# Kernel optimization log

Hardware: AMD Instinct MI355X
Metric: run time of the kernel (lower is better)

## Reference

```python
import jax, jax.numpy as jnp
import numpy as np

B, DEC_T, ENC_T = 64, 128, 1024
H, ENC_D, ATTN, VOCAB = 512, 512, 512, 128


def setup_inputs() -> dict:
    key = jax.random.key(0)
    ks = jax.random.split(key, 12)
    s = 0.05
    return {
        "inputs": jax.random.randint(ks[0], (B, DEC_T), 0, 127),
        "encoder_outputs": jax.random.normal(ks[1], (B, ENC_T, ENC_D), jnp.float32),
        "embedding": jax.random.normal(ks[2], (VOCAB, H), jnp.float32) * s,
        "w_ih": jax.random.normal(ks[3], (3 * H, H + ENC_D), jnp.float32) * s,
        "w_hh": jax.random.normal(ks[4], (3 * H, H), jnp.float32) * s,
        "b_ih": jnp.zeros((3 * H,), jnp.float32),
        "b_hh": jnp.zeros((3 * H,), jnp.float32),
        "attn_wq": jax.random.normal(ks[5], (ATTN, H), jnp.float32) * s,
        "attn_wv": jax.random.normal(ks[6], (ATTN, ENC_D), jnp.float32) * s,
        "attn_conv_w": jax.random.normal(ks[7], (ATTN, 1, 3), jnp.float32) * s,
        "attn_conv_b": jnp.zeros((ATTN,), jnp.float32),
        "attn_bias": jnp.zeros((ATTN,), jnp.float32),
        "attn_v": jax.random.normal(ks[8], (ATTN,), jnp.float32) * s,
        "fc_w": jax.random.normal(ks[9], (VOCAB, H + ENC_D), jnp.float32) * s,
        "fc_b": jnp.zeros((VOCAB,), jnp.float32),
    }


def reference(inputs, encoder_outputs, embedding, w_ih, w_hh, b_ih, b_hh,
              attn_wq, attn_wv, attn_conv_w, attn_conv_b, attn_bias, attn_v,
              fc_w, fc_b):
    emb = embedding[inputs]  # (B, dec_T, H); no eos in inputs so filter is identity
    # precompute encoder value projection once (reused every step)
    enc_proj = jnp.einsum('bte,ae->bta', encoder_outputs, attn_wv)  # (B, enc_T, A)

    def gru_step(h, x):
        gi = x @ w_ih.T + b_ih  # (B, 3H)
        gh = h @ w_hh.T + b_hh
        r = jax.nn.sigmoid(gi[:, :H] + gh[:, :H])
        z = jax.nn.sigmoid(gi[:, H:2 * H] + gh[:, H:2 * H])
        n = jnp.tanh(gi[:, 2 * H:] + r * gh[:, 2 * H:])
        return (1.0 - z) * n + z * h

    def step(carry, x_t):
        h, context, attn_w = carry
        rnn_in = jnp.concatenate([x_t, context], axis=1)  # (B, H+enc_D)
        h = gru_step(h, rnn_in)  # output == new hidden for 1-layer GRU
        # location-aware attention: conv over previous attention weights
        conv = jax.lax.conv_general_dilated(
            attn_w[:, None, :], attn_conv_w, (1,), ((1, 1),),
            dimension_numbers=('NCH', 'OIH', 'NCH'))  # (B, A, enc_T)
        conv_feat = conv.transpose(0, 2, 1) + attn_conv_b  # (B, enc_T, A)
        q = h @ attn_wq.T  # (B, A)
        e = jnp.tanh(q[:, None, :] + enc_proj + conv_feat + attn_bias)
        score = jnp.einsum('bta,a->bt', e, attn_v)  # (B, enc_T)
        attn_w = jax.nn.softmax(score, axis=-1)
        context = jnp.einsum('bt,bte->be', attn_w, encoder_outputs)  # (B, enc_D)
        out_cat = jnp.concatenate([h, context], axis=1)  # (B, H+enc_D)
        pred = jax.nn.log_softmax(out_cat @ fc_w.T + fc_b, axis=-1)  # (B, V)
        return (h, context, attn_w), (pred, attn_w, out_cat)

    init = (jnp.zeros((B, H), emb.dtype),
            jnp.zeros((B, ENC_D), emb.dtype),
            jnp.zeros((B, ENC_T), emb.dtype))
    _, (y, aw, oc) = jax.lax.scan(step, init, emb.transpose(1, 0, 2))
    # back to batch-major: (B, dec_T, *)
    return (y.transpose(1, 0, 2), aw.transpose(1, 0, 2), oc.transpose(1, 0, 2))
```

## Files before the change

kernel.cpp:

```cpp
#include <hip/hip_runtime.h>
#include <stdint.h>

#define BB 64
#define SS 128
#define EE 1024
#define HH 512
#define DD 512
#define AA 512
#define VV 128
#define KX 1536
#define NC 2048

#define AW_OFF ((size_t)BB*SS*VV)
#define OC_OFF (AW_OFF + (size_t)BB*SS*EE)

typedef unsigned short u16;

__device__ __forceinline__ float sigmoid_f(float x){
  return __builtin_amdgcn_rcpf(1.f + __expf(-x));
}
__device__ __forceinline__ float tanh_f(float x){
  float e = __expf(2.f*x);
  return 1.f - 2.f*__builtin_amdgcn_rcpf(e + 1.f);
}
__device__ __forceinline__ u16 f2bf(float f){
  uint32_t u = __float_as_uint(f);
  return (u16)((u + 0x7fffu + ((u>>16)&1u)) >> 16);
}

__global__ void k_build(const float* __restrict__ w_ih, const float* __restrict__ w_hh,
                        const float* __restrict__ b_ih, const float* __restrict__ b_hh,
                        const float* __restrict__ wq,   const float* __restrict__ wv,
                        const float* __restrict__ fc_w,
                        float* __restrict__ Wbig, float* __restrict__ wqT,
                        float* __restrict__ wvT,  float* __restrict__ fcT,
                        float* __restrict__ bias_big){
  int i = blockIdx.x*256 + threadIdx.x;
  const int NW = KX*NC;
  if (i < NW){
    int k = i >> 11, c = i & (NC-1);
    float v;
    if (c < 1024)      v = (k < 1024) ? w_ih[c*1024 + k] : w_hh[c*512 + (k-1024)];
    else if (c < 1536) v = (k < 1024) ? w_ih[c*1024 + k] : 0.f;
    else               v = (k >= 1024) ? w_hh[(c-512)*512 + (k-1024)] : 0.f;
    Wbig[i] = v; return;
  }
  i -= NW;
  if (i < 512*512){ int j = i >> 9, a = i & 511; wqT[i] = wq[a*512 + j]; return; }
  i -= 512*512;
  if (i < 512*512){ int e = i >> 9, a = i & 511; wvT[i] = wv[a*512 + e]; return; }
  i -= 512*512;
  if (i < 1024*128){ int k = i >> 7, v = i & 127; fcT[i] = fc_w[v*1024 + k]; return; }
  i -= 1024*128;
  if (i < NC){
    float bv;
    if (i < 1024)      bv = b_ih[i] + b_hh[i];
    else if (i < 1536) bv = b_ih[i];
    else               bv = b_hh[i - 512];
    bias_big[i] = bv;
  }
}

__global__ __launch_bounds__(256) void k_encp(const float* __restrict__ enc,
                                              const float* __restrict__ wvT,
                                              const float* __restrict__ abias,
                                              const float* __restrict__ convb,
                                              u16* __restrict__ encp){
  __shared__ float As[64][36];
  __shared__ float Bs[32][68];
  int tid = threadIdx.x;
  int r0 = blockIdx.x * 64;
  int a0 = blockIdx.y * 64;
  float4 acc[4];
  #pragma unroll
  for (int r = 0; r < 4; ++r) acc[r] = make_float4(0.f,0.f,0.f,0.f);
  int rl = tid >> 2, kl0 = (tid & 3) * 8;
  int kl2 = tid >> 3, al0 = (tid & 7) * 8;
  int br = (tid >> 4) * 4, cc = (tid & 15) * 4;
  for (int kk = 0; kk < 512; kk += 32){
    float4 av0 = *(const float4*)&enc[(size_t)(r0+rl)*512 + kk + kl0];
    float4 av1 = *(const float4*)&enc[(size_t)(r0+rl)*512 + kk + kl0 + 4];
    float4 bv0 = *(const float4*)&wvT[(size_t)(kk+kl2)*512 + a0 + al0];
    float4 bv1 = *(const float4*)&wvT[(size_t)(kk+kl2)*512 + a0 + al0 + 4];
    __syncthreads();
    *(float4*)&As[rl][kl0]     = av0;
    *(float4*)&As[rl][kl0+4]   = av1;
    *(float4*)&Bs[kl2][al0]    = bv0;
    *(float4*)&Bs[kl2][al0+4]  = bv1;
    __syncthreads();
    #pragma unroll
    for (int i = 0; i < 32; ++i){
      float4 b4 = *(const float4*)&Bs[i][cc];
      float x0 = As[br][i], x1 = As[br+1][i], x2 = As[br+2][i], x3 = As[br+3][i];
      acc[0].x += x0*b4.x; acc[0].y += x0*b4.y; acc[0].z += x0*b4.z; acc[0].w += x0*b4.w;
      acc[1].x += x1*b4.x; acc[1].y += x1*b4.y; acc[1].z += x1*b4.z; acc[1].w += x1*b4.w;
      acc[2].x += x2*b4.x; acc[2].y += x2*b4.y; acc[2].z += x2*b4.z; acc[2].w += x2*b4.w;
      acc[3].x += x3*b4.x; acc[3].y += x3*b4.y; acc[3].z += x3*b4.z; acc[3].w += x3*b4.w;
    }
  }
  int a = a0 + cc;
  float b0f = abias[a]   + convb[a];
  float b1f = abias[a+1] + convb[a+1];
  float b2f_ = abias[a+2] + convb[a+2];
  float b3f = abias[a+3] + convb[a+3];
  #pragma unroll
  for (int r = 0; r < 4; ++r){
    size_t row = (size_t)(r0 + br + r);
    ushort4 pk;
    pk.x = f2bf(acc[r].x + b0f);
    pk.y = f2bf(acc[r].y + b1f);
    pk.z = f2bf(acc[r].z + b2f_);
    pk.w = f2bf(acc[r].w + b3f);
    *(ushort4*)&encp[row*512 + a] = pk;
  }
}

__global__ __launch_bounds__(256) void k_encbf(const float* __restrict__ enc,
                                               u16* __restrict__ enc_bf){
  size_t i = ((size_t)blockIdx.x*256 + threadIdx.x) * 4;
  float4 v = *(const float4*)&enc[i];
  ushort4 pk;
  pk.x = f2bf(v.x); pk.y = f2bf(v.y); pk.z = f2bf(v.z); pk.w = f2bf(v.w);
  *(ushort4*)&enc_bf[i] = pk;
}

__global__ __launch_bounds__(256) void k_ggemm_fc(const int* __restrict__ inputs,
                                                  const float* __restrict__ emb,
                                                  const float* __restrict__ ctxp,
                                                  const float* __restrict__ h,
                                                  const float* __restrict__ Wbig,
                                                  float* __restrict__ Gp,
                                                  const float* __restrict__ fcT,
                                                  const float* __restrict__ fc_b,
                                                  float* __restrict__ out,
                                                  int s, int gemm_nb, int sfc){
  int tid = threadIdx.x;
  if ((int)blockIdx.x < gemm_nb){
    __shared__ float Xs[64][36];
    __shared__ float Ws[32][68];
    int bid = blockIdx.x;
    int c0 = (bid & 31) * 64;
    int kc = bid >> 5;
    int kbase = kc * 192;
    float4 acc[4];
    #pragma unroll
    for (int r = 0; r < 4; ++r) acc[r] = make_float4(0.f,0.f,0.f,0.f);
    int bl = tid >> 2, kl0 = (tid & 3) * 8;
    int kw = tid >> 3, cl0 = (tid & 7) * 8;
    int br = (tid >> 4) * 4, cc = (tid & 15) * 4;
    const float* emb_b = emb + (size_t)inputs[bl*SS + s]*HH;
    bool t0 = (s == 0);
    for (int kk = 0; kk < 192; kk += 32){
      float xv[8];
      #pragma unroll
      for (int u = 0; u < 8; ++u){
        int kg = kbase + kk + kl0 + u;
        float v;
        if (kg < 512)       v = emb_b[kg];
        else if (kg < 1024){
          if (t0) v = 0.f;
          else {
            int d = kg - 512;
            v = ctxp[(size_t)(0*64+bl)*512 + d] + ctxp[(size_t)(1*64+bl)*512 + d]
              + ctxp[(size_t)(2*64+bl)*512 + d] + ctxp[(size_t)(3*64+bl)*512 + d];
          }
        }
        else                v = t0 ? 0.f : h[bl*512 + kg - 1024];
        xv[u] = v;
      }
      float4 w1 = *(const float4*)&Wbig[(size_t)(kbase+kk+kw)*NC + c0 + cl0];
      float4 w2 = *(const float4*)&Wbig[(size_t)(kbase+kk+kw)*NC + c0 + cl0 + 4];
      __syncthreads();
      *(float4*)&Xs[bl][kl0]   = make_float4(xv[0],xv[1],xv[2],xv[3]);
      *(float4*)&Xs[bl][kl0+4] = make_float4(xv[4],xv[5],xv[6],xv[7]);
      *(float4*)&Ws[kw][cl0]   = w1;
      *(float4*)&Ws[kw][cl0+4] = w2;
      __syncthreads();
      #pragma unroll
      for (int i = 0; i < 32; ++i){
        float4 b4 = *(const float4*)&Ws[i][cc];
        float x0 = Xs[br][i], x1 = Xs[br+1][i], x2 = Xs[br+2][i], x3 = Xs[br+3][i];
        acc[0].x += x0*b4.x; acc[0].y += x0*b4.y; acc[0].z += x0*b4.z; acc[0].w += x0*b4.w;
        acc[1].x += x1*b4.x; acc[1].y += x1*b4.y; acc[1].z += x1*b4.z; acc[1].w += x1*b4.w;
        acc[2].x += x2*b4.x; acc[2].y += x2*b4.y; acc[2].z += x2*b4.z; acc[2].w += x2*b4.w;
        acc[3].x += x3*b4.x; acc[3].y += x3*b4.y; acc[3].z += x3*b4.z; acc[3].w += x3*b4.w;
      }
    }
    #pragma unroll
    for (int r = 0; r < 4; ++r)
      *(float4*)&Gp[(size_t)(kc*64 + br + r)*NC + c0 + cc] = acc[r];
  } else {
    if (sfc < 0) return;
    __shared__ float oc_l[1024];
    __shared__ float lp[2][128];
    __shared__ float l_l[128];
    int b = blockIdx.x - gemm_nb;
    oc_l[tid]       = h[b*512 + tid];
    oc_l[tid + 256] = h[b*512 + tid + 256];
    int d0 = tid*2;
    float a0 = 0.f, a1 = 0.f;
    #pragma unroll
    for (int cc2 = 0; cc2 < 4; ++cc2){
      float2 p2 = *(const float2*)&ctxp[(size_t)(cc2*64 + b)*512 + d0];
      a0 += p2.x; a1 += p2.y;
    }
    oc_l[512 + d0]     = a0;
    oc_l[512 + d0 + 1] = a1;
    size_t oco = OC_OFF + (size_t)(b*SS + sfc)*1024 + 512 + d0;
    out[oco]     = a0;
    out[oco + 1] = a1;
    __syncthreads();
    int v = tid & 127, half = tid >> 7;
    float acc = 0.f;
    #pragma unroll 8
    for (int k = 0; k < 512; ++k)
      acc += oc_l[half*512 + k] * fcT[(size_t)(half*512 + k)*128 + v];
    lp[half][v] = acc;
    __syncthreads();
    if (tid < 128) l_l[tid] = lp[0][tid] + lp[1][tid] + fc_b[tid];
    __syncthreads();
    if (tid < 128){
      float m = -1e30f;
      for (int i = 0; i < 128; ++i) m = fmaxf(m, l_l[i]);
      float sm = 0.f;
      for (int i = 0; i < 128; ++i) sm += __expf(l_l[i] - m);
      out[(size_t)(b*SS + sfc)*VV + tid] = l_l[tid] - m - __logf(sm);
    }
  }
}

__global__ __launch_bounds__(256) void k_gate_q(const float* __restrict__ Gp,
                                                const float* __restrict__ bias_big,
                                                float* __restrict__ h,
                                                const float* __restrict__ wqT,
                                                float* __restrict__ qp,
                                                float* __restrict__ out, int s){
  __shared__ float h_l[512];
  int tid = threadIdx.x;
  int jt = blockIdx.x, bt = blockIdx.y;
  bool t0 = (s == 0);
  #pragma unroll
  for (int it = 0; it < 2; ++it){
    int item = tid + it*256;
    int bi = item >> 6, jl = item & 63;
    int b = bt*8 + bi, j = jt*64 + jl;
    float s0=0.f, s1=0.f, s2=0.f, s3=0.f;
    #pragma unroll
    for (int kc = 0; kc < 8; ++kc){
      const float* g = Gp + (size_t)(kc*64 + b)*NC;
      s0 += g[j]; s1 += g[512+j]; s2 += g[1024+j]; s3 += g[1536+j];
    }
    float r = sigmoid_f(s0 + bias_big[j]);
    float z = sigmoid_f(s1 + bias_big[512+j]);
    float n = tanh_f(s2 + bias_big[1024+j] + r*(s3 + bias_big[1536+j]));
    float hold = t0 ? 0.f : h[b*512 + j];
    float hn = (1.f - z)*n + z*hold;
    h_l[item] = hn;
    h[b*512 + j] = hn;
    out[OC_OFF + (size_t)(b*SS + s)*1024 + j] = hn;
  }
  __syncthreads();
  int a0 = tid*2;
  float2 acc8[8];
  #pragma unroll
  for (int bi = 0; bi < 8; ++bi) acc8[bi] = make_float2(0.f, 0.f);
  for (int j = 0; j < 64; ++j){
    float2 w = *(const float2*)&wqT[(size_t)(jt*64 + j)*512 + a0];
    #pragma unroll
    for (int bi = 0; bi < 8; ++bi){
      float hv = h_l[bi*64 + j];
      acc8[bi].x += hv*w.x; acc8[bi].y += hv*w.y;
    }
  }
  #pragma unroll
  for (int bi = 0; bi < 8; ++bi)
    *(float2*)&qp[(size_t)(jt*64 + bt*8 + bi)*512 + a0] = acc8[bi];
}

__global__ __launch_bounds__(1024) void k_score(const float* __restrict__ qp,
                                                const float* __restrict__ attn_v,
                                                const float* __restrict__ conv_w,
                                                const u16* __restrict__ encp,
                                                const float* __restrict__ out_aw,
                                                float* __restrict__ score, int s){
  __shared__ float q_l[512], v_l[512], c0_l[512], c1_l[512], c2_l[512];
  int tid = threadIdx.x;
  int b = blockIdx.y, et = blockIdx.x;
  if (tid < 512){
    float qq = 0.f;
    #pragma unroll
    for (int jt = 0; jt < 8; ++jt) qq += qp[(size_t)(jt*64 + b)*512 + tid];
    q_l[tid]  = qq;
    v_l[tid]  = attn_v[tid];
    c0_l[tid] = conv_w[tid*3 + 0];
    c1_l[tid] = conv_w[tid*3 + 1];
    c2_l[tid] = conv_w[tid*3 + 2];
  }
  __syncthreads();
  int wave = tid >> 6, lane = tid & 63;
  float q8[8], v8[8], c08[8], c18[8], c28[8];
  #pragma unroll
  for (int i = 0; i < 8; ++i){
    int a = lane*8 + i;
    q8[i] = q_l[a]; v8[i] = v_l[a]; c08[i] = c0_l[a]; c18[i] = c1_l[a]; c28[i] = c2_l[a];
  }
  const float* awrow = out_aw + AW_OFF + (size_t)(b*SS + (s-1))*EE;
  #pragma unroll
  for (int eu = 0; eu < 8; ++eu){
    int e = et*128 + wave*8 + eu;
    float wl = 0.f, wc = 0.f, wr = 0.f;
    if (s > 0){
      wc = awrow[e];
      wl = (e > 0)    ? awrow[e-1] : 0.f;
      wr = (e < EE-1) ? awrow[e+1] : 0.f;
    }
    uint4 pk = *(const uint4*)(encp + ((size_t)(b*EE + e)*512 + lane*8));
    uint32_t ua[4] = {pk.x, pk.y, pk.z, pk.w};
    float acc = 0.f;
    #pragma unroll
    for (int p = 0; p < 4; ++p){
      float plo = __uint_as_float(ua[p] << 16);
      float phi = __uint_as_float(ua[p] & 0xffff0000u);
      int i = p*2;
      float v0 = q8[i]   + plo + c08[i]*wl   + c18[i]*wc   + c28[i]*wr;
      acc += tanh_f(v0) * v8[i];
      float v1 = q8[i+1] + phi + c08[i+1]*wl + c18[i+1]*wc + c28[i+1]*wr;
      acc += tanh_f(v1) * v8[i+1];
    }
    #pragma unroll
    for (int off = 32; off; off >>= 1) acc += __shfl_xor(acc, off, 64);
    if (lane == 0) score[b*EE + e] = acc;
  }
}

__global__ __launch_bounds__(512) void k_soft_ctx(const float* __restrict__ score,
                                                  const u16* __restrict__ enc_bf,
                                                  float* __restrict__ ctxp,
                                                  float* __restrict__ out, int s){
  __shared__ float s_l[1024];
  __shared__ float red[512];
  __shared__ float w_l[256];
  __shared__ float redc[8][512];
  int tid = threadIdx.x;
  int c = blockIdx.x, b = blockIdx.y;
  float lv0 = score[b*EE + tid];
  float lv1 = score[b*EE + 512 + tid];
  s_l[tid] = lv0; s_l[512 + tid] = lv1;
  float m = fmaxf(lv0, lv1);
  red[tid] = m; __syncthreads();
  for (int st = 256; st > 0; st >>= 1){
    if (tid < st) red[tid] = fmaxf(red[tid], red[tid+st]);
    __syncthreads();
  }
  m = red[0]; __syncthreads();
  float sm = __expf(lv0 - m) + __expf(lv1 - m);
  red[tid] = sm; __syncthreads();
  for (int st = 256; st > 0; st >>= 1){
    if (tid < st) red[tid] += red[tid+st];
    __syncthreads();
  }
  float rS = __builtin_amdgcn_rcpf(red[0]);
  if (tid < 256){
    int e = c*256 + tid;
    float w = __expf(s_l[e] - m) * rS;
    w_l[tid] = w;
    out[AW_OFF + (size_t)(b*SS + s)*EE + e] = w;
  }
  __syncthreads();
  int es = tid >> 6, lane = tid & 63;
  int d0 = lane * 8;
  float acc8[8];
  #pragma unroll
  for (int i = 0; i < 8; ++i) acc8[i] = 0.f;
  #pragma unroll 4
  for (int i = 0; i < 32; ++i){
    int e_loc = es*32 + i;
    int e = c*256 + e_loc;
    uint4 pk = *(const uint4*)(enc_bf + ((size_t)b*EE + e)*512 + d0);
    float w = w_l[e_loc];
    uint32_t ua[4] = {pk.x, pk.y, pk.z, pk.w};
    #pragma unroll
    for (int p = 0; p < 4; ++p){
      acc8[p*2]   += w * __uint_as_float(ua[p] << 16);
      acc8[p*2+1] += w * __uint_as_float(ua[p] & 0xffff0000u);
    }
  }
  #pragma unroll
  for (int i = 0; i < 8; ++i) redc[es][d0 + i] = acc8[i];
  __syncthreads();
  if (tid < 128){
    int d = tid * 4;
    float4 t = make_float4(0.f,0.f,0.f,0.f);
    #pragma unroll
    for (int e2 = 0; e2 < 8; ++e2){
      float4 r4 = *(const float4*)&redc[e2][d];
      t.x += r4.x; t.y += r4.y; t.z += r4.z; t.w += r4.w;
    }
    *(float4*)&ctxp[(size_t)(c*64 + b)*512 + d] = t;
  }
}

extern "C" void kernel_launch(void* const* d_in, const int* in_sizes, int n_in,
                              void* d_out, int out_size, void* d_ws, size_t ws_size,
                              hipStream_t stream){
  (void)in_sizes; (void)n_in; (void)out_size; (void)ws_size;
  const int*   inputs = (const int*)d_in[0];
  const float* enc    = (const float*)d_in[1];
  const float* emb    = (const float*)d_in[2];
  const float* w_ih   = (const float*)d_in[3];
  const float* w_hh   = (const float*)d_in[4];
  const float* b_ih   = (const float*)d_in[5];
  const float* b_hh   = (const float*)d_in[6];
  const float* wq     = (const float*)d_in[7];
  const float* wv     = (const float*)d_in[8];
  const float* convw  = (const float*)d_in[9];
  const float* convb  = (const float*)d_in[10];
  const float* abias  = (const float*)d_in[11];
  const float* av     = (const float*)d_in[12];
  const float* fcw    = (const float*)d_in[13];
  const float* fcb    = (const float*)d_in[14];
  float* out = (float*)d_out;

  char* p = (char*)d_ws;
  auto alloc = [&](size_t bytes)->char*{
    char* r = p; p += (bytes + 255) & ~(size_t)255; return r;
  };
  u16*   encp   = (u16*)  alloc((size_t)BB*EE*AA*2);
  u16*   enc_bf = (u16*)  alloc((size_t)BB*EE*DD*2);
  float* Wbig   = (float*)alloc((size_t)KX*NC*4);
  float* wqT    = (float*)alloc((size_t)512*512*4);
  float* wvT    = (float*)alloc((size_t)512*512*4);
  float* fcT    = (float*)alloc((size_t)1024*128*4);
  float* biasb  = (float*)alloc((size_t)NC*4);
  float* hbuf   = (float*)alloc((size_t)BB*HH*4);
  float* Gp     = (float*)alloc((size_t)8*BB*NC*4);
  float* qp     = (float*)alloc((size_t)8*BB*AA*4);
  float* score  = (float*)alloc((size_t)BB*EE*4);
  float* ctxp   = (float*)alloc((size_t)4*BB*DD*4);

  int total0 = KX*NC + 512*512 + 512*512 + 1024*128 + NC;
  k_build<<<(total0 + 255)/256, 256, 0, stream>>>(w_ih, w_hh, b_ih, b_hh, wq, wv, fcw,
                                                  Wbig, wqT, wvT, fcT, biasb);
  k_encp<<<dim3(1024, 8), 256, 0, stream>>>(enc, wvT, abias, convb, encp);
  k_encbf<<<(BB*EE*DD/4 + 255)/256, 256, 0, stream>>>(enc, enc_bf);

  for (int s = 0; s < SS; ++s){
    int sfc = s - 1;
    int grid = (sfc >= 0) ? 320 : 256;
    k_ggemm_fc<<<grid, 256, 0, stream>>>(inputs, emb, ctxp, hbuf, Wbig, Gp,
                                         fcT, fcb, out, s, 256, sfc);
    k_gate_q<<<dim3(8, 8), 256, 0, stream>>>(Gp, biasb, hbuf, wqT, qp, out, s);
    k_score<<<dim3(8, 64), 1024, 0, stream>>>(qp, av, convw, encp, out, score, s);
    k_soft_ctx<<<dim3(4, 64), 512, 0, stream>>>(score, enc_bf, ctxp, out, s);
  }
  k_ggemm_fc<<<64, 256, 0, stream>>>(inputs, emb, ctxp, hbuf, Wbig, Gp,
                                     fcT, fcb, out, 0, 0, SS-1);
}
```

Baseline: 10.04 ms.

## Fuse attention scoring with softmax-context using deferred normalization

Merges the score kernel and the softmax/context kernel into one per-step kernel. Each block writes unnormalized exp(scores), per-block partial sums and partial context vectors. Normalization by the reciprocal sum is deferred to consumers: the next step's GEMM, the FC blocks, and the conv over previous attention weights. This removes one launch per decoder step, the score buffer round-trip and the block-wide max/sum reductions. In exchange it drops max-subtraction in the exponent, which relies on scores staying small, and moves the attention-weight output write one step later, so a new tail kernel is needed for the final step.

New measurement: 12.55 ms. 25.0% more time.

```diff
diff --git a/kernel.cpp b/kernel.cpp
--- a/kernel.cpp
+++ b/kernel.cpp
@@ -127,21 +127,31 @@
 __global__ __launch_bounds__(256) void k_ggemm_fc(const int* __restrict__ inputs,
                                                   const float* __restrict__ emb,
                                                   const float* __restrict__ ctxp,
+                                                  const float* __restrict__ sump,
                                                   const float* __restrict__ h,
                                                   const float* __restrict__ Wbig,
                                                   float* __restrict__ Gp,
                                                   const float* __restrict__ fcT,
                                                   const float* __restrict__ fc_b,
+                                                  float* __restrict__ rs_buf,
                                                   float* __restrict__ out,
                                                   int s, int gemm_nb, int sfc){
   int tid = threadIdx.x;
   if ((int)blockIdx.x < gemm_nb){
     __shared__ float Xs[64][36];
     __shared__ float Ws[32][68];
+    __shared__ float rs_l[64];
     int bid = blockIdx.x;
     int c0 = (bid & 31) * 64;
     int kc = bid >> 5;
     int kbase = kc * 192;
+    bool t0 = (s == 0);
+    if (!t0 && tid < 64){
+      float ssum = 0.f;
+      #pragma unroll
+      for (int p2 = 0; p2 < 8; ++p2) ssum += sump[p2*64 + tid];
+      rs_l[tid] = __builtin_amdgcn_rcpf(ssum);
+    }
     float4 acc[4];
     #pragma unroll
     for (int r = 0; r < 4; ++r) acc[r] = make_float4(0.f,0.f,0.f,0.f);
@@ -149,7 +159,7 @@
     int kw = tid >> 3, cl0 = (tid & 7) * 8;
     int br = (tid >> 4) * 4, cc = (tid & 15) * 4;
     const float* emb_b = emb + (size_t)inputs[bl*SS + s]*HH;
-    bool t0 = (s == 0);
+    __syncthreads();
     for (int kk = 0; kk < 192; kk += 32){
       float xv[8];
       #pragma unroll
@@ -161,8 +171,10 @@
           if (t0) v = 0.f;
           else {
             int d = kg - 512;
-            v = ctxp[(size_t)(0*64+bl)*512 + d] + ctxp[(size_t)(1*64+bl)*512 + d]
-              + ctxp[(size_t)(2*64+bl)*512 + d] + ctxp[(size_t)(3*64+bl)*512 + d];
+            float t = 0.f;
+            #pragma unroll
+            for (int p2 = 0; p2 < 8; ++p2) t += ctxp[(size_t)(p2*64+bl)*512 + d];
+            v = t * rs_l[bl];
           }
         }
         else                v = t0 ? 0.f : h[bl*512 + kg - 1024];
@@ -195,15 +207,21 @@
     __shared__ float lp[2][128];
     __shared__ float l_l[128];
     int b = blockIdx.x - gemm_nb;
+    float ssum = 0.f;
+    #pragma unroll
+    for (int p2 = 0; p2 < 8; ++p2) ssum += sump[p2*64 + b];
+    float rs = __builtin_amdgcn_rcpf(ssum);
+    if (tid == 0) rs_buf[b] = rs;
     oc_l[tid]       = h[b*512 + tid];
     oc_l[tid + 256] = h[b*512 + tid + 256];
     int d0 = tid*2;
     float a0 = 0.f, a1 = 0.f;
     #pragma unroll
-    for (int cc2 = 0; cc2 < 4; ++cc2){
-      float2 p2 = *(const float2*)&ctxp[(size_t)(cc2*64 + b)*512 + d0];
-      a0 += p2.x; a1 += p2.y;
-    }
+    for (int cc2 = 0; cc2 < 8; ++cc2){
+      float2 p2v = *(const float2*)&ctxp[(size_t)(cc2*64 + b)*512 + d0];
+      a0 += p2v.x; a1 += p2v.y;
+    }
+    a0 *= rs; a1 *= rs;
     oc_l[512 + d0]     = a0;
     oc_l[512 + d0 + 1] = a1;
     size_t oco = OC_OFF + (size_t)(b*SS + sfc)*1024 + 512 + d0;
@@ -277,16 +295,23 @@
     *(float2*)&qp[(size_t)(jt*64 + bt*8 + bi)*512 + a0] = acc8[bi];
 }
 
-__global__ __launch_bounds__(1024) void k_score(const float* __restrict__ qp,
-                                                const float* __restrict__ attn_v,
-                                                const float* __restrict__ conv_w,
-                                                const u16* __restrict__ encp,
-                                                const float* __restrict__ out_aw,
-                                                float* __restrict__ score, int s){
+__global__ __launch_bounds__(512) void k_score_ctx(const float* __restrict__ qp,
+                                                   const float* __restrict__ attn_v,
+                                                   const float* __restrict__ conv_w,
+                                                   const u16* __restrict__ encp,
+                                                   const u16* __restrict__ enc_bf,
+                                                   const float* __restrict__ expsc_prev,
+                                                   float* __restrict__ expsc_cur,
+                                                   const float* __restrict__ rs_buf,
+                                                   float* __restrict__ sump,
+                                                   float* __restrict__ ctxp,
+                                                   float* __restrict__ out, int s){
   __shared__ float q_l[512], v_l[512], c0_l[512], c1_l[512], c2_l[512];
+  __shared__ float ew_l[128];
+  __shared__ float redc[8][512];
   int tid = threadIdx.x;
-  int b = blockIdx.y, et = blockIdx.x;
-  if (tid < 512){
+  int et = blockIdx.x, b = blockIdx.y;
+  {
     float qq = 0.f;
     #pragma unroll
     for (int jt = 0; jt < 8; ++jt) qq += qp[(size_t)(jt*64 + b)*512 + tid];
@@ -304,15 +329,17 @@
     int a = lane*8 + i;
     q8[i] = q_l[a]; v8[i] = v_l[a]; c08[i] = c0_l[a]; c18[i] = c1_l[a]; c28[i] = c2_l[a];
   }
-  const float* awrow = out_aw + AW_OFF + (size_t)(b*SS + (s-1))*EE;
-  #pragma unroll
-  for (int eu = 0; eu < 8; ++eu){
-    int e = et*128 + wave*8 + eu;
+  float rs_prev = (s > 0) ? rs_buf[b] : 0.f;
+  const float* prev = expsc_prev + (size_t)b*EE;
+  #pragma unroll 2
+  for (int i = 0; i < 16; ++i){
+    int e_loc = wave*16 + i;
+    int e = et*128 + e_loc;
     float wl = 0.f, wc = 0.f, wr = 0.f;
     if (s > 0){
-      wc = awrow[e];
-      wl = (e > 0)    ? awrow[e-1] : 0.f;
-      wr = (e < EE-1) ? awrow[e+1] : 0.f;
+      wc = prev[e] * rs_prev;
+      wl = (e > 0)    ? prev[e-1]*rs_prev : 0.f;
+      wr = (e < EE-1) ? prev[e+1]*rs_prev : 0.f;
     }
     uint4 pk = *(const uint4*)(encp + ((size_t)(b*EE + e)*512 + lane*8));
     uint32_t ua[4] = {pk.x, pk.y, pk.z, pk.w};
@@ -321,63 +348,38 @@
     for (int p = 0; p < 4; ++p){
       float plo = __uint_as_float(ua[p] << 16);
       float phi = __uint_as_float(ua[p] & 0xffff0000u);
-      int i = p*2;
-      float v0 = q8[i]   + plo + c08[i]*wl   + c18[i]*wc   + c28[i]*wr;
-      acc += tanh_f(v0) * v8[i];
-      float v1 = q8[i+1] + phi + c08[i+1]*wl + c18[i+1]*wc + c28[i+1]*wr;
-      acc += tanh_f(v1) * v8[i+1];
+      int ii = p*2;
+      float v0 = q8[ii]   + plo + c08[ii]*wl   + c18[ii]*wc   + c28[ii]*wr;
+      acc += tanh_f(v0) * v8[ii];
+      float v1 = q8[ii+1] + phi + c08[ii+1]*wl + c18[ii+1]*wc + c28[ii+1]*wr;
+      acc += tanh_f(v1) * v8[ii+1];
     }
     #pragma unroll
     for (int off = 32; off; off >>= 1) acc += __shfl_xor(acc, off, 64);
-    if (lane == 0) score[b*EE + e] = acc;
-  }
-}
-
-__global__ __launch_bounds__(512) void k_soft_ctx(const float* __restrict__ score,
-                                                  const u16* __restrict__ enc_bf,
-                                                  float* __restrict__ ctxp,
-                                                  float* __restrict__ out, int s){
-  __shared__ float s_l[1024];
-  __shared__ float red[512];
-  __shared__ float w_l[256];
-  __shared__ float redc[8][512];
-  int tid = threadIdx.x;
-  int c = blockIdx.x, b = blockIdx.y;
-  float lv0 = score[b*EE + tid];
-  float lv1 = score[b*EE + 512 + tid];
-  s_l[tid] = lv0; s_l[512 + tid] = lv1;
-  float m = fmaxf(lv0, lv1);
-  red[tid] = m; __syncthreads();
-  for (int st = 256; st > 0; st >>= 1){
-    if (tid < st) red[tid] = fmaxf(red[tid], red[tid+st]);
-    __syncthreads();
-  }
-  m = red[0]; __syncthreads();
-  float sm = __expf(lv0 - m) + __expf(lv1 - m);
-  red[tid] = sm; __syncthreads();
-  for (int st = 256; st > 0; st >>= 1){
-    if (tid < st) red[tid] += red[tid+st];
-    __syncthreads();
-  }
-  float rS = __builtin_amdgcn_rcpf(red[0]);
-  if (tid < 256){
-    int e = c*256 + tid;
-    float w = __expf(s_l[e] - m) * rS;
-    w_l[tid] = w;
-    out[AW_OFF + (size_t)(b*SS + s)*EE + e] = w;
-  }
-  __syncthreads();
-  int es = tid >> 6, lane = tid & 63;
+    if (lane == 0){
+      float ew = __expf(acc);
+      ew_l[e_loc] = ew;
+      expsc_cur[(size_t)b*EE + e] = ew;
+      if (s > 0) out[AW_OFF + (size_t)(b*SS + (s-1))*EE + e] = wc;
+    }
+  }
+  __syncthreads();
+  if (tid < 64){
+    float t2 = ew_l[tid] + ew_l[tid + 64];
+    #pragma unroll
+    for (int off = 32; off; off >>= 1) t2 += __shfl_xor(t2, off, 64);
+    if (tid == 0) sump[et*64 + b] = t2;
+  }
   int d0 = lane * 8;
   float acc8[8];
   #pragma unroll
   for (int i = 0; i < 8; ++i) acc8[i] = 0.f;
-  #pragma unroll 4
-  for (int i = 0; i < 32; ++i){
-    int e_loc = es*32 + i;
-    int e = c*256 + e_loc;
-    uint4 pk = *(const uint4*)(enc_bf + ((size_t)b*EE + e)*512 + d0);
-    float w = w_l[e_loc];
+  #pragma unroll 2
+  for (int i = 0; i < 16; ++i){
+    int e_loc = wave*16 + i;
+    int e = et*128 + e_loc;
+    uint4 pk = *(const uint4*)(enc_bf + ((size_t)(b*EE + e)*512 + d0));
+    float w = ew_l[e_loc];
     uint32_t ua[4] = {pk.x, pk.y, pk.z, pk.w};
     #pragma unroll
     for (int p = 0; p < 4; ++p){
@@ -386,7 +388,7 @@
     }
   }
   #pragma unroll
-  for (int i = 0; i < 8; ++i) redc[es][d0 + i] = acc8[i];
+  for (int i = 0; i < 8; ++i) redc[wave][d0 + i] = acc8[i];
   __syncthreads();
   if (tid < 128){
     int d = tid * 4;
@@ -396,7 +398,62 @@
       float4 r4 = *(const float4*)&redc[e2][d];
       t.x += r4.x; t.y += r4.y; t.z += r4.z; t.w += r4.w;
     }
-    *(float4*)&ctxp[(size_t)(c*64 + b)*512 + d] = t;
+    *(float4*)&ctxp[(size_t)(et*64 + b)*512 + d] = t;
+  }
+}
+
+__global__ __launch_bounds__(256) void k_tail(const float* __restrict__ h,
+                                              const float* __restrict__ ctxp,
+                                              const float* __restrict__ sump,
+                                              const float* __restrict__ expsc,
+                                              const float* __restrict__ fcT,
+                                              const float* __restrict__ fc_b,
+                                              float* __restrict__ out){
+  __shared__ float oc_l[1024];
+  __shared__ float lp[2][128];
+  __shared__ float l_l[128];
+  int tid = threadIdx.x, b = blockIdx.x;
+  const int sfc = SS - 1;
+  float ssum = 0.f;
+  #pragma unroll
+  for (int p2 = 0; p2 < 8; ++p2) ssum += sump[p2*64 + b];
+  float rs = __builtin_amdgcn_rcpf(ssum);
+  #pragma unroll
+  for (int i = 0; i < 4; ++i){
+    int e = i*256 + tid;
+    out[AW_OFF + (size_t)(b*SS + sfc)*EE + e] = expsc[(size_t)b*EE + e] * rs;
+  }
+  oc_l[tid]       = h[b*512 + tid];
+  oc_l[tid + 256] = h[b*512 + tid + 256];
+  int d0 = tid*2;
+  float a0 = 0.f, a1 = 0.f;
+  #pragma unroll
+  for (int cc2 = 0; cc2 < 8; ++cc2){
+    float2 p2v = *(const float2*)&ctxp[(size_t)(cc2*64 + b)*512 + d0];
+    a0 += p2v.x; a1 += p2v.y;
+  }
+  a0 *= rs; a1 *= rs;
+  oc_l[512 + d0]     = a0;
+  oc_l[512 + d0 + 1] = a1;
+  size_t oco = OC_OFF + (size_t)(b*SS + sfc)*1024 + 512 + d0;
+  out[oco]     = a0;
+  out[oco + 1] = a1;
+  __syncthreads();
+  int v = tid & 127, half = tid >> 7;
+  float acc = 0.f;
+  #pragma unroll 8
+  for (int k = 0; k < 512; ++k)
+    acc += oc_l[half*512 + k] * fcT[(size_t)(half*512 + k)*128 + v];
+  lp[half][v] = acc;
+  __syncthreads();
+  if (tid < 128) l_l[tid] = lp[0][tid] + lp[1][tid] + fc_b[tid];
+  __syncthreads();
+  if (tid < 128){
+    float m = -1e30f;
+    for (int i = 0; i < 128; ++i) m = fmaxf(m, l_l[i]);
+    float sm = 0.f;
+    for (int i = 0; i < 128; ++i) sm += __expf(l_l[i] - m);
+    out[(size_t)(b*SS + sfc)*VV + tid] = l_l[tid] - m - __logf(sm);
   }
 }
 
@@ -435,8 +492,11 @@
   float* hbuf   = (float*)alloc((size_t)BB*HH*4);
   float* Gp     = (float*)alloc((size_t)8*BB*NC*4);
   float* qp     = (float*)alloc((size_t)8*BB*AA*4);
-  float* score  = (float*)alloc((size_t)BB*EE*4);
-  float* ctxp   = (float*)alloc((size_t)4*BB*DD*4);
+  float* exps0  = (float*)alloc((size_t)BB*EE*4);
+  float* exps1  = (float*)alloc((size_t)BB*EE*4);
+  float* sump   = (float*)alloc((size_t)8*BB*4);
+  float* ctxp   = (float*)alloc((size_t)8*BB*DD*4);
+  float* rs_buf = (float*)alloc((size_t)BB*4);
 
   int total0 = KX*NC + 512*512 + 512*512 + 1024*128 + NC;
   k_build<<<(total0 + 255)/256, 256, 0, stream>>>(w_ih, w_hh, b_ih, b_hh, wq, wv, fcw,
@@ -447,12 +507,14 @@
   for (int s = 0; s < SS; ++s){
     int sfc = s - 1;
     int grid = (sfc >= 0) ? 320 : 256;
-    k_ggemm_fc<<<grid, 256, 0, stream>>>(inputs, emb, ctxp, hbuf, Wbig, Gp,
-                                         fcT, fcb, out, s, 256, sfc);
+    float* e_prev = (s & 1) ? exps0 : exps1;
+    float* e_cur  = (s & 1) ? exps1 : exps0;
+    k_ggemm_fc<<<grid, 256, 0, stream>>>(inputs, emb, ctxp, sump, hbuf, Wbig, Gp,
+                                         fcT, fcb, rs_buf, out, s, 256, sfc);
     k_gate_q<<<dim3(8, 8), 256, 0, stream>>>(Gp, biasb, hbuf, wqT, qp, out, s);
-    k_score<<<dim3(8, 64), 1024, 0, stream>>>(qp, av, convw, encp, out, score, s);
-    k_soft_ctx<<<dim3(4, 64), 512, 0, stream>>>(score, enc_bf, ctxp, out, s);
-  }
-  k_ggemm_fc<<<64, 256, 0, stream>>>(inputs, emb, ctxp, hbuf, Wbig, Gp,
-                                     fcT, fcb, out, 0, 0, SS-1);
-}
+    k_score_ctx<<<dim3(8, 64), 512, 0, stream>>>(qp, av, convw, encp, enc_bf,
+                                                 e_prev, e_cur, rs_buf, sump, ctxp,
+                                                 out, s);
+  }
+  k_tail<<<64, 256, 0, stream>>>(hbuf, ctxp, sump, exps1, fcT, fcb, out);
+}
```
